# Optimization experiments

Hardware: AMD Instinct MI355X
Metric: run time of the kernel (lower is better)

Reference implementation:

```python
import jax, jax.numpy as jnp
import numpy as np


def setup_inputs() -> dict:
    key = jax.random.key(0)
    ks = jax.random.split(key, 5)
    N, C, H, W = 4, 256, 64, 64
    fan_scale = 1.0 / np.sqrt(C)  # kaiming-ish scale for 1x1 conv weights
    x = jax.random.normal(ks[0], (N, C, H, W), dtype=jnp.float32)
    Wq = jax.random.normal(ks[1], (C, C), dtype=jnp.float32) * fan_scale
    Wk = jax.random.normal(ks[2], (C, C), dtype=jnp.float32) * fan_scale
    Wv = jax.random.normal(ks[3], (C, C), dtype=jnp.float32) * fan_scale
    bq = jnp.zeros((C,), dtype=jnp.float32)
    bk = jnp.zeros((C,), dtype=jnp.float32)
    bv = jnp.zeros((C,), dtype=jnp.float32)
    gamma = jax.random.uniform(ks[4], (1,), dtype=jnp.float32)
    return {"x": x, "Wq": Wq, "bq": bq, "Wk": Wk, "bk": bk, "Wv": Wv, "bv": bv, "gamma": gamma}


def reference(x, Wq, bq, Wk, bk, Wv, bv, gamma):
    # x: (N, C, H, W); 1x1 convs are channel-mixing matmuls.
    N, C, H, W = x.shape
    HW = H * W
    xf = x.reshape(N, C, HW)
    q = jnp.einsum('oc,ncl->nol', Wq, xf) + bq[None, :, None]  # (N, C, HW)
    k = jnp.einsum('oc,ncl->nol', Wk, xf) + bk[None, :, None]
    v = jnp.einsum('oc,ncl->nol', Wv, xf) + bv[None, :, None]
    # spatial mode: energy = softmax(Q^T K) over last dim (no 1/sqrt(d) scaling)
    energy = jax.nn.softmax(jnp.einsum('nci,ncj->nij', q, k), axis=-1)  # (N, HW, HW)
    # att[n,c,i] = sum_j v[n,c,j] * energy[n,i,j]  (bmm(value, energy^T))
    att = jnp.einsum('ncj,nij->nci', v, energy)  # (N, C, HW)
    # in_channels == out_channels -> residual is identity
    out = x + gamma[0] * att.reshape(N, C, H, W)
    return out
```

## Files before the change

kernel.cpp:

```cpp
#include <hip/hip_runtime.h>

typedef unsigned short ushort_t;
typedef unsigned int u32;
typedef _Float16 f16;
typedef f16 f16x8 __attribute__((ext_vector_type(8)));
typedef f16 f16x2 __attribute__((ext_vector_type(2)));
typedef ushort_t u16x8 __attribute__((ext_vector_type(8)));
typedef float f32x4 __attribute__((ext_vector_type(4)));
typedef float f32x16 __attribute__((ext_vector_type(16)));

#define C_DIM 256
#define HW 4096
#define CHW (C_DIM*HW)
#define L2E 1.4426950408889634f

__device__ __align__(16) f16 g_xbT[4 * CHW];
__device__ __align__(16) f16 g_q[4 * CHW];
__device__ __align__(16) f16 g_k[4 * CHW];
__device__ __align__(16) f16 g_v[4 * CHW];
__device__ __align__(16) f16 g_opart[16 * CHW];
__device__ __align__(16) float g_ml[16 * 2 * HW];

__device__ __forceinline__ float bf2f(ushort_t h) {
    union { u32 u; float f; } v; v.u = ((u32)h) << 16; return v.f;
}
__device__ __forceinline__ ushort_t f2bf(float f) {
    union { float f; u32 u; } v; v.f = f;
    u32 r = v.u + 0x7FFF + ((v.u >> 16) & 1);
    return (ushort_t)(r >> 16);
}
__device__ __forceinline__ float fin0(float v) {
    return (v > -1e30f && v < 1e30f) ? v : 0.f;
}
__device__ __forceinline__ f16 sf16(float v) {
    return (f16)((v > -1e4f && v < 1e4f) ? v : 0.f);
}
__device__ __forceinline__ void gl2lds16(const f16* g, f16* l) {
    __builtin_amdgcn_global_load_lds(
        (const __attribute__((address_space(1))) u32*)g,
        (__attribute__((address_space(3))) u32*)l, 16, 0, 0);
}
__device__ __forceinline__ int probe_mode(const void* p) {
    int lane = threadIdx.x & 63;
    float v = fabsf(bf2f(((const ushort_t*)p)[lane]));
    v = (v < 1e6f) ? v : 1e6f;
#pragma unroll
    for (int d = 1; d < 64; d <<= 1) v += __shfl_xor(v, d, 64);
    return (v * (1.f / 64.f) > 100.f) ? 1 : 0;
}

__global__ void k_sentinel(ushort_t* out, int n) {
    int i = blockIdx.x * 256 + threadIdx.x;
    if (i < n) out[i] = f2bf(777.f);
}

__global__ __launch_bounds__(256) void k_transpose(const void* __restrict__ xv) {
    __shared__ f16 t[64][66];
    int mode = probe_mode(xv);
    int n = blockIdx.z, c0 = blockIdx.y * 64, l0 = blockIdx.x * 64;
    int tid = threadIdx.x;
    f16* ob = g_xbT + n * CHW;
    int lq = (tid & 15) * 4;
    int cl = tid >> 4;
    if (mode == 0) {
        const ushort_t* xb = (const ushort_t*)xv + n * CHW;
#pragma unroll
        for (int p = 0; p < 4; ++p) {
            int c = cl + 16 * p;
            ushort4 v = *(const ushort4*)(xb + (c0 + c) * HW + l0 + lq);
            t[lq + 0][c] = sf16(bf2f(v.x));
            t[lq + 1][c] = sf16(bf2f(v.y));
            t[lq + 2][c] = sf16(bf2f(v.z));
            t[lq + 3][c] = sf16(bf2f(v.w));
        }
    } else {
        const float* xb = (const float*)xv + n * CHW;
#pragma unroll
        for (int p = 0; p < 4; ++p) {
            int c = cl + 16 * p;
            float4 v = *(const float4*)(xb + (c0 + c) * HW + l0 + lq);
            t[lq + 0][c] = sf16(v.x);
            t[lq + 1][c] = sf16(v.y);
            t[lq + 2][c] = sf16(v.z);
            t[lq + 3][c] = sf16(v.w);
        }
    }
    __syncthreads();
    int c2 = (tid & 31) * 2;
    int lr = tid >> 5;
#pragma unroll
    for (int p = 0; p < 8; ++p) {
        int l = lr + 8 * p;
        u32 pair = *(const u32*)&t[l][c2];
        *(u32*)(ob + (l0 + l) * C_DIM + c0 + c2) = pair;
    }
}

__global__ __launch_bounds__(256) void k_proj(
    const void* __restrict__ Wq, const void* __restrict__ bq,
    const void* __restrict__ Wk, const void* __restrict__ bk,
    const void* __restrict__ Wv, const void* __restrict__ bv)
{
    __shared__ __align__(16) f16 lds_x[128 * 64];
    __shared__ __align__(16) f16 lds_w[128 * 64];
    int l0 = blockIdx.x * 128;
    int og0 = blockIdx.y * 128;
    int n = blockIdx.z;
    int mat = og0 >> 8;
    int om0 = og0 & 255;
    const void* W = (mat == 0) ? Wq : (mat == 1) ? Wk : Wv;
    const void* bias = (mat == 0) ? bq : (mat == 1) ? bk : bv;
    int mode = probe_mode(W);
    int tid = threadIdx.x, w = tid >> 6, lane = tid & 63;
    int quad = lane >> 4, l16 = lane & 15;
    const f16* xb = g_xbT + n * CHW;

    f32x4 acc[2][8];
#pragma unroll
    for (int a = 0; a < 2; a++)
#pragma unroll
        for (int b = 0; b < 8; b++) acc[a][b] = f32x4{0.f, 0.f, 0.f, 0.f};

    for (int ch = 0; ch < 4; ++ch) {
        int cc0 = ch * 64;
        f16x8 xs[4], wsr[4];
#pragma unroll
        for (int ti = 0; ti < 4; ++ti) {
            int s = (w * 4 + ti) * 64 + lane;
            int row = s >> 3, gp = s & 7;
            xs[ti] = *(const f16x8*)(xb + (l0 + row) * C_DIM + cc0 + gp * 8);
            f16x8 h;
            if (mode == 0) {
                u16x8 wv = *(const u16x8*)((const ushort_t*)W + (om0 + row) * C_DIM + cc0 + gp * 8);
#pragma unroll
                for (int e = 0; e < 8; e++) h[e] = sf16(bf2f(wv[e]));
            } else {
                const float* wf = (const float*)W + (om0 + row) * C_DIM + cc0 + gp * 8;
#pragma unroll
                for (int e = 0; e < 8; e++) h[e] = sf16(wf[e]);
            }
            wsr[ti] = h;
        }
        __syncthreads();
#pragma unroll
        for (int ti = 0; ti < 4; ++ti) {
            int s = (w * 4 + ti) * 64 + lane;
            int row = s >> 3, gp = s & 7;
            int pos = gp ^ (row & 7);
            *(f16x8*)(lds_x + (row * 8 + pos) * 8) = xs[ti];
            *(f16x8*)(lds_w + (row * 8 + pos) * 8) = wsr[ti];
        }
        __syncthreads();
#pragma unroll
        for (int ks = 0; ks < 2; ++ks) {
            f16x8 af[2];
#pragma unroll
            for (int mt = 0; mt < 2; ++mt) {
                int row = w * 32 + mt * 16 + l16;
                int g = ks * 4 + quad;
                int pos = g ^ (row & 7);
                af[mt] = *(const f16x8*)(lds_x + (row * 8 + pos) * 8);
            }
#pragma unroll
            for (int nt = 0; nt < 8; ++nt) {
                int rowo = nt * 16 + l16;
                int g = ks * 4 + quad;
                int pos = g ^ (rowo & 7);
                f16x8 bfv = *(const f16x8*)(lds_w + (rowo * 8 + pos) * 8);
                if (mat < 2) {
                    acc[0][nt] = __builtin_amdgcn_mfma_f32_16x16x32_f16(af[0], bfv, acc[0][nt], 0, 0, 0);
                    acc[1][nt] = __builtin_amdgcn_mfma_f32_16x16x32_f16(af[1], bfv, acc[1][nt], 0, 0, 0);
                } else {
                    acc[0][nt] = __builtin_amdgcn_mfma_f32_16x16x32_f16(bfv, af[0], acc[0][nt], 0, 0, 0);
                    acc[1][nt] = __builtin_amdgcn_mfma_f32_16x16x32_f16(bfv, af[1], acc[1][nt], 0, 0, 0);
                }
            }
        }
        __syncthreads();
    }

    auto loadb = [&](int i) -> float {
        return mode ? ((const float*)bias)[i] : bf2f(((const ushort_t*)bias)[i]);
    };
    if (mat < 2) {
        f16* T = ((mat == 0) ? g_q : g_k) + n * CHW;
        float bvv[8];
#pragma unroll
        for (int nt = 0; nt < 8; nt++) bvv[nt] = loadb(om0 + nt * 16 + l16);
#pragma unroll
        for (int mt = 0; mt < 2; mt++)
#pragma unroll
            for (int nt = 0; nt < 8; nt++)
#pragma unroll
                for (int r = 0; r < 4; r++) {
                    int l = l0 + w * 32 + mt * 16 + quad * 4 + r;
                    int o = om0 + nt * 16 + l16;
                    T[l * C_DIM + o] = sf16(acc[mt][nt][r] + bvv[nt]);
                }
    } else {
        f16* T = g_v + n * CHW;
#pragma unroll
        for (int mt = 0; mt < 2; mt++)
#pragma unroll
            for (int nt = 0; nt < 8; nt++)
#pragma unroll
                for (int r = 0; r < 4; r++) {
                    int o = om0 + nt * 16 + quad * 4 + r;
                    int l = l0 + w * 32 + mt * 16 + l16;
                    T[o * HW + l] = sf16(acc[mt][nt][r] + loadb(o));
                }
    }
}

__device__ __forceinline__ f16x8 pack_pfrag(const float* p, int h) {
    union PK { u32 u; f16x2 h2; } t0, t1, t2, t3;
    t0.h2 = f16x2{(f16)p[0], (f16)p[1]};
    t1.h2 = f16x2{(f16)p[2], (f16)p[3]};
    t2.h2 = f16x2{(f16)p[4], (f16)p[5]};
    t3.h2 = f16x2{(f16)p[6], (f16)p[7]};
    u32 sa = __shfl_xor(t0.u, 32, 64);
    u32 sb = __shfl_xor(t1.u, 32, 64);
    u32 sc = __shfl_xor(t2.u, 32, 64);
    u32 sd = __shfl_xor(t3.u, 32, 64);
    union RW { u32 w[4]; f16x8 v; } r;
    r.w[0] = h ? sc : t0.u;
    r.w[1] = h ? sd : t1.u;
    r.w[2] = h ? t2.u : sa;
    r.w[3] = h ? t3.u : sb;
    return r.v;
}

__global__ __launch_bounds__(256, 2) void k_attn() {
    __shared__ __align__(16) f16 smem[32768];
    f16* kbuf = smem;
    f16* vbuf = smem + 16384;

    int bid = blockIdx.x;
    int x8 = bid & 7;
    int n = x8 >> 1, jhi = x8 & 1;
    int rest = bid >> 3;
    int jlo = rest & 1;
    int i0 = (rest >> 1) * 128;
    int jq = jhi * 2 + jlo;
    int tid = threadIdx.x, w = tid >> 6, lane = tid & 63;
    int j5 = lane & 31, h = lane >> 5;

    const f16* Qb = g_q + n * CHW;
    const f16* Kb = g_k + n * CHW;
    const f16* Vb = g_v + n * CHW;

    f16x8 qf[16];
    {
        const f16* qrow = Qb + (i0 + w * 32 + j5) * C_DIM + h * 8;
#pragma unroll
        for (int ck = 0; ck < 16; ++ck)
            qf[ck] = *(const f16x8*)(qrow + ck * 16);
    }

    int k_lane = h * 256 + j5 * 8;
    int v_lane = h * 2048 + j5 * 8;

    const f16* ksrc = Kb + (jq * 1024 + j5) * C_DIM + (w * 2 + h) * 8;
    const f16* vsrc = Vb + tid * HW + jq * 1024;
    int dst_w = w * 512;

    f32x16 o_acc[8];
#pragma unroll
    for (int ct = 0; ct < 8; ++ct)
#pragma unroll
        for (int r = 0; r < 16; ++r) o_acc[ct][r] = 0.f;

    float m_ = -1e30f, l_ = 0.f, al_prev = 1.f;
    f16x8 pf0 = {}, pf1 = {};

#pragma unroll
    for (int s = 0; s < 4; ++s) gl2lds16(ksrc + s * 64, kbuf + s * 2048 + dst_w);
    ksrc += 32 * C_DIM;
    __syncthreads();

    for (int it = 0; it < 32; ++it) {
        int kcur = it & 1;
        if (it < 31) {
#pragma unroll
            for (int s = 0; s < 4; ++s)
                gl2lds16(ksrc + s * 64, kbuf + (kcur ^ 1) * 8192 + s * 2048 + dst_w);
            ksrc += 32 * C_DIM;
        }
#pragma unroll
        for (int s = 0; s < 4; ++s)
            gl2lds16(vsrc + s * 8, vbuf + (it & 1) * 8192 + s * 2048 + dst_w);
        vsrc += 32;

        if (it > 0 && __any(al_prev < 1.f)) {
#pragma unroll
            for (int ct = 0; ct < 8; ++ct)
#pragma unroll
                for (int r = 0; r < 16; ++r) o_acc[ct][r] *= al_prev;
        }

        const f16* kb = kbuf + kcur * 8192 + k_lane;
        f32x16 sa, sb;
#pragma unroll
        for (int r = 0; r < 16; ++r) { sa[r] = 0.f; sb[r] = 0.f; }
        __builtin_amdgcn_s_setprio(1);
        if (it > 0) {
            const f16* vb = vbuf + ((it - 1) & 1) * 8192 + v_lane;
#pragma unroll
            for (int ck = 0; ck < 16; ++ck) {
                f16x8 kf = *(const f16x8*)(kb + ck * 512);
                if (ck & 1) sb = __builtin_amdgcn_mfma_f32_32x32x16_f16(kf, qf[ck], sb, 0, 0, 0);
                else        sa = __builtin_amdgcn_mfma_f32_32x32x16_f16(kf, qf[ck], sa, 0, 0, 0);
                f16x8 vf = *(const f16x8*)(vb + (ck & 1) * 4096 + (ck >> 1) * 256);
                o_acc[ck >> 1] = __builtin_amdgcn_mfma_f32_32x32x16_f16(
                    vf, (ck & 1) ? pf1 : pf0, o_acc[ck >> 1], 0, 0, 0);
            }
        } else {
#pragma unroll
            for (int ck = 0; ck < 16; ++ck) {
                f16x8 kf = *(const f16x8*)(kb + ck * 512);
                if (ck & 1) sb = __builtin_amdgcn_mfma_f32_32x32x16_f16(kf, qf[ck], sb, 0, 0, 0);
                else        sa = __builtin_amdgcn_mfma_f32_32x32x16_f16(kf, qf[ck], sa, 0, 0, 0);
            }
        }
        __builtin_amdgcn_s_setprio(0);
        f32x16 st;
#pragma unroll
        for (int r = 0; r < 16; ++r) st[r] = sa[r] + sb[r];

        float mx0 = fmaxf(fmaxf(st[0], st[1]), fmaxf(st[2], st[3]));
        float mx1 = fmaxf(fmaxf(st[4], st[5]), fmaxf(st[6], st[7]));
        float mx2 = fmaxf(fmaxf(st[8], st[9]), fmaxf(st[10], st[11]));
        float mx3 = fmaxf(fmaxf(st[12], st[13]), fmaxf(st[14], st[15]));
        float smax = fmaxf(fmaxf(mx0, mx1), fmaxf(mx2, mx3));
        smax = fmaxf(smax, __shfl_xor(smax, 32, 64));
        float mq = __builtin_ceilf(smax * 0.125f) * 8.f;
        float mn = fmaxf(m_, mq);
        float al = __builtin_amdgcn_exp2f((m_ - mn) * L2E);
        float nl = -mn * L2E;
        float p[16];
#pragma unroll
        for (int r = 0; r < 16; ++r)
            p[r] = __builtin_amdgcn_exp2f(st[r] * L2E + nl);
        float a0 = (p[0] + p[1]) + (p[2] + p[3]);
        float a1 = (p[4] + p[5]) + (p[6] + p[7]);
        float a2 = (p[8] + p[9]) + (p[10] + p[11]);
        float a3 = (p[12] + p[13]) + (p[14] + p[15]);
        float rs = (a0 + a1) + (a2 + a3);
        m_ = mn;
        l_ = l_ * al + rs;
        al_prev = al;
        pf0 = pack_pfrag(p, h);
        pf1 = pack_pfrag(p + 8, h);

        __syncthreads();
    }

    {
        if (__any(al_prev < 1.f)) {
#pragma unroll
            for (int ct = 0; ct < 8; ++ct)
#pragma unroll
                for (int r = 0; r < 16; ++r) o_acc[ct][r] *= al_prev;
        }
        const f16* vb = vbuf + 8192 + v_lane;
#pragma unroll
        for (int ct = 0; ct < 8; ++ct) {
            f16x8 v0 = *(const f16x8*)(vb + ct * 256);
            f16x8 v1 = *(const f16x8*)(vb + 4096 + ct * 256);
            o_acc[ct] = __builtin_amdgcn_mfma_f32_32x32x16_f16(v0, pf0, o_acc[ct], 0, 0, 0);
            o_acc[ct] = __builtin_amdgcn_mfma_f32_32x32x16_f16(v1, pf1, o_acc[ct], 0, 0, 0);
        }
    }

    l_ += __shfl_xor(l_, 32, 64);

    int slot = jq * 4 + n;
    int i_out = i0 + w * 32 + j5;
    if (h == 0) {
        g_ml[(slot * 2 + 0) * HW + i_out] = m_;
        g_ml[(slot * 2 + 1) * HW + i_out] = l_;
    }
    float inv = (l_ > 1e-30f) ? 1.f / l_ : 0.f;
    f16* ob = g_opart + slot * CHW + i_out;
#pragma unroll
    for (int ct = 0; ct < 8; ++ct) {
        int cbase = ct * 32 + 4 * h;
#pragma unroll
        for (int r = 0; r < 16; ++r) {
            int c = cbase + (r & 3) + 8 * (r >> 2);
            ob[c * HW] = (f16)(o_acc[ct][r] * inv);
        }
    }
}

__global__ __launch_bounds__(256) void k_combine(
    const void* __restrict__ xv, const void* __restrict__ gv, void* __restrict__ outv)
{
    int mode = probe_mode(xv);
    float gam = fin0(mode ? ((const float*)gv)[0] : bf2f(((const ushort_t*)gv)[0]));
    int n = blockIdx.y;
    int off = blockIdx.x * 2048 + threadIdx.x * 8;
    int i = off & (HW - 1);

    u16x8 op[4];
    float ms[4][8], ls[4][8];
#pragma unroll
    for (int s = 0; s < 4; ++s) {
        int slot = s * 4 + n;
        op[s] = *(const u16x8*)((const ushort_t*)g_opart + slot * CHW + off);
        float4 mA = *(const float4*)&g_ml[(slot * 2 + 0) * HW + i];
        float4 mB = *(const float4*)&g_ml[(slot * 2 + 0) * HW + i + 4];
        float4 lA = *(const float4*)&g_ml[(slot * 2 + 1) * HW + i];
        float4 lB = *(const float4*)&g_ml[(slot * 2 + 1) * HW + i + 4];
        ms[s][0]=mA.x; ms[s][1]=mA.y; ms[s][2]=mA.z; ms[s][3]=mA.w;
        ms[s][4]=mB.x; ms[s][5]=mB.y; ms[s][6]=mB.z; ms[s][7]=mB.w;
        ls[s][0]=lA.x; ls[s][1]=lA.y; ls[s][2]=lA.z; ls[s][3]=lA.w;
        ls[s][4]=lB.x; ls[s][5]=lB.y; ls[s][6]=lB.z; ls[s][7]=lB.w;
    }

    float o[8];
#pragma unroll
    for (int e = 0; e < 8; ++e) {
        float m = fmaxf(fmaxf(ms[0][e], ms[1][e]), fmaxf(ms[2][e], ms[3][e]));
        float num = 0.f, den = 0.f;
#pragma unroll
        for (int s = 0; s < 4; ++s) {
            float wgt = __builtin_amdgcn_exp2f((ms[s][e] - m) * L2E) * ls[s][e];
            union { ushort_t u; f16 h; } cv; cv.u = (ushort_t)op[s][e];
            num += wgt * (float)cv.h;
            den += wgt;
        }
        o[e] = (den > 1e-30f) ? num / den : 0.f;
    }

    if (mode == 0) {
        u16x8 xp = *(const u16x8*)((const ushort_t*)xv + n * CHW + off);
        u16x8 res;
#pragma unroll
        for (int e = 0; e < 8; ++e)
            res[e] = f2bf(fin0(bf2f((ushort_t)xp[e]) + gam * o[e]));
        *(u16x8*)((ushort_t*)outv + n * CHW + off) = res;
    } else {
        const float* xb = (const float*)xv + n * CHW + off;
        float* outb = (float*)outv + n * CHW + off;
        float4 xA = *(const float4*)xb;
        float4 xB = *(const float4*)(xb + 4);
        float4 rA, rB;
        rA.x = fin0(xA.x + gam * o[0]); rA.y = fin0(xA.y + gam * o[1]);
        rA.z = fin0(xA.z + gam * o[2]); rA.w = fin0(xA.w + gam * o[3]);
        rB.x = fin0(xB.x + gam * o[4]); rB.y = fin0(xB.y + gam * o[5]);
        rB.z = fin0(xB.z + gam * o[6]); rB.w = fin0(xB.w + gam * o[7]);
        *(float4*)outb = rA;
        *(float4*)(outb + 4) = rB;
    }
}

extern "C" void kernel_launch(void* const* d_in, const int* in_sizes, int n_in,
                              void* d_out, int out_size, void* d_ws, size_t ws_size,
                              hipStream_t stream) {
    (void)d_ws; (void)ws_size;
    bool ok = (n_in == 8) &&
              in_sizes[0] == 4 * CHW &&
              in_sizes[1] == C_DIM * C_DIM && in_sizes[2] == C_DIM &&
              in_sizes[3] == C_DIM * C_DIM && in_sizes[4] == C_DIM &&
              in_sizes[5] == C_DIM * C_DIM && in_sizes[6] == C_DIM &&
              in_sizes[7] == 1 && out_size == 4 * CHW;
    if (!ok) {
        hipLaunchKernelGGL(k_sentinel, dim3((out_size + 255) / 256), dim3(256), 0, stream,
                           (ushort_t*)d_out, out_size);
        return;
    }
    hipLaunchKernelGGL(k_transpose, dim3(64, 4, 4), dim3(256), 0, stream, d_in[0]);
    hipLaunchKernelGGL(k_proj, dim3(32, 6, 4), dim3(256), 0, stream,
                       d_in[1], d_in[2], d_in[3], d_in[4], d_in[5], d_in[6]);
    hipLaunchKernelGGL(k_attn, dim3(512), dim3(256), 0, stream);
    hipLaunchKernelGGL(k_combine, dim3(CHW / 2048, 4), dim3(256), 0, stream,
                       d_in[0], d_in[7], d_out);
}
```

Before: 239.3 us.

## Restructure flash-attention loop with split barriers and explicit vmcnt waits

Replaces the single end-of-iteration __syncthreads with two explicit s_barrier points, each using a partial s_waitcnt vmcnt so newer global-to-LDS K/V copies can stay in flight while older ones are consumed. The PV MFMAs move out of the interleaved QK loop into a separate block placed after the mid-iteration barrier, and the last iteration is peeled. The aim is to stop draining all outstanding loads at every barrier and so overlap memory traffic with compute better. It relies on hand-counted vmcnt values and sched_barriers, which are fragile if the number of loads per thread changes, and it loses the previous interleaving of QK and PV MFMAs.

```diff
diff --git a/kernel.cpp b/kernel.cpp
--- a/kernel.cpp
+++ b/kernel.cpp
@@ -276,56 +276,61 @@
 #pragma unroll
     for (int s = 0; s < 4; ++s) gl2lds16(ksrc + s * 64, kbuf + s * 2048 + dst_w);
     ksrc += 32 * C_DIM;
-    __syncthreads();
-
-    for (int it = 0; it < 32; ++it) {
+    asm volatile("s_waitcnt vmcnt(0)" ::: "memory");
+    __builtin_amdgcn_s_barrier();
+    __builtin_amdgcn_sched_barrier(0);
+
+    for (int it = 0; it < 31; ++it) {
         int kcur = it & 1;
-        if (it < 31) {
-#pragma unroll
-            for (int s = 0; s < 4; ++s)
-                gl2lds16(ksrc + s * 64, kbuf + (kcur ^ 1) * 8192 + s * 2048 + dst_w);
-            ksrc += 32 * C_DIM;
-        }
 #pragma unroll
         for (int s = 0; s < 4; ++s)
-            gl2lds16(vsrc + s * 8, vbuf + (it & 1) * 8192 + s * 2048 + dst_w);
+            gl2lds16(ksrc + s * 64, kbuf + (kcur ^ 1) * 8192 + s * 2048 + dst_w);
+        ksrc += 32 * C_DIM;
+        __builtin_amdgcn_sched_barrier(0);
+#pragma unroll
+        for (int s = 0; s < 4; ++s)
+            gl2lds16(vsrc + s * 8, vbuf + kcur * 8192 + s * 2048 + dst_w);
         vsrc += 32;
-
-        if (it > 0 && __any(al_prev < 1.f)) {
-#pragma unroll
-            for (int ct = 0; ct < 8; ++ct)
-#pragma unroll
-                for (int r = 0; r < 16; ++r) o_acc[ct][r] *= al_prev;
-        }
+        __builtin_amdgcn_sched_barrier(0);
 
         const f16* kb = kbuf + kcur * 8192 + k_lane;
         f32x16 sa, sb;
 #pragma unroll
         for (int r = 0; r < 16; ++r) { sa[r] = 0.f; sb[r] = 0.f; }
         __builtin_amdgcn_s_setprio(1);
-        if (it > 0) {
-            const f16* vb = vbuf + ((it - 1) & 1) * 8192 + v_lane;
-#pragma unroll
-            for (int ck = 0; ck < 16; ++ck) {
-                f16x8 kf = *(const f16x8*)(kb + ck * 512);
-                if (ck & 1) sb = __builtin_amdgcn_mfma_f32_32x32x16_f16(kf, qf[ck], sb, 0, 0, 0);
-                else        sa = __builtin_amdgcn_mfma_f32_32x32x16_f16(kf, qf[ck], sa, 0, 0, 0);
-                f16x8 vf = *(const f16x8*)(vb + (ck & 1) * 4096 + (ck >> 1) * 256);
-                o_acc[ck >> 1] = __builtin_amdgcn_mfma_f32_32x32x16_f16(
-                    vf, (ck & 1) ? pf1 : pf0, o_acc[ck >> 1], 0, 0, 0);
-            }
-        } else {
-#pragma unroll
-            for (int ck = 0; ck < 16; ++ck) {
-                f16x8 kf = *(const f16x8*)(kb + ck * 512);
-                if (ck & 1) sb = __builtin_amdgcn_mfma_f32_32x32x16_f16(kf, qf[ck], sb, 0, 0, 0);
-                else        sa = __builtin_amdgcn_mfma_f32_32x32x16_f16(kf, qf[ck], sa, 0, 0, 0);
-            }
+#pragma unroll
+        for (int ck = 0; ck < 16; ++ck) {
+            f16x8 kf = *(const f16x8*)(kb + ck * 512);
+            if (ck & 1) sb = __builtin_amdgcn_mfma_f32_32x32x16_f16(kf, qf[ck], sb, 0, 0, 0);
+            else        sa = __builtin_amdgcn_mfma_f32_32x32x16_f16(kf, qf[ck], sa, 0, 0, 0);
         }
         __builtin_amdgcn_s_setprio(0);
         f32x16 st;
 #pragma unroll
         for (int r = 0; r < 16; ++r) st[r] = sa[r] + sb[r];
+
+        asm volatile("s_waitcnt vmcnt(8)" ::: "memory");
+        __builtin_amdgcn_s_barrier();
+        __builtin_amdgcn_sched_barrier(0);
+
+        if (it > 0) {
+            if (__any(al_prev < 1.f)) {
+#pragma unroll
+                for (int ct = 0; ct < 8; ++ct)
+#pragma unroll
+                    for (int r = 0; r < 16; ++r) o_acc[ct][r] *= al_prev;
+            }
+            const f16* vb = vbuf + (kcur ^ 1) * 8192 + v_lane;
+            __builtin_amdgcn_s_setprio(1);
+#pragma unroll
+            for (int ct = 0; ct < 8; ++ct) {
+                f16x8 v0 = *(const f16x8*)(vb + ct * 256);
+                f16x8 v1 = *(const f16x8*)(vb + 4096 + ct * 256);
+                o_acc[ct] = __builtin_amdgcn_mfma_f32_32x32x16_f16(v0, pf0, o_acc[ct], 0, 0, 0);
+                o_acc[ct] = __builtin_amdgcn_mfma_f32_32x32x16_f16(v1, pf1, o_acc[ct], 0, 0, 0);
+            }
+            __builtin_amdgcn_s_setprio(0);
+        }
 
         float mx0 = fmaxf(fmaxf(st[0], st[1]), fmaxf(st[2], st[3]));
         float mx1 = fmaxf(fmaxf(st[4], st[5]), fmaxf(st[6], st[7]));
@@ -352,10 +357,84 @@
         pf0 = pack_pfrag(p, h);
         pf1 = pack_pfrag(p + 8, h);
 
-        __syncthreads();
+        asm volatile("s_waitcnt vmcnt(4)" ::: "memory");
+        __builtin_amdgcn_s_barrier();
+        __builtin_amdgcn_sched_barrier(0);
     }
 
     {
+#pragma unroll
+        for (int s = 0; s < 4; ++s)
+            gl2lds16(vsrc + s * 8, vbuf + 8192 + s * 2048 + dst_w);
+        __builtin_amdgcn_sched_barrier(0);
+
+        const f16* kb = kbuf + 8192 + k_lane;
+        f32x16 sa, sb;
+#pragma unroll
+        for (int r = 0; r < 16; ++r) { sa[r] = 0.f; sb[r] = 0.f; }
+        __builtin_amdgcn_s_setprio(1);
+#pragma unroll
+        for (int ck = 0; ck < 16; ++ck) {
+            f16x8 kf = *(const f16x8*)(kb + ck * 512);
+            if (ck & 1) sb = __builtin_amdgcn_mfma_f32_32x32x16_f16(kf, qf[ck], sb, 0, 0, 0);
+            else        sa = __builtin_amdgcn_mfma_f32_32x32x16_f16(kf, qf[ck], sa, 0, 0, 0);
+        }
+        __builtin_amdgcn_s_setprio(0);
+        f32x16 st;
+#pragma unroll
+        for (int r = 0; r < 16; ++r) st[r] = sa[r] + sb[r];
+
+        asm volatile("s_waitcnt vmcnt(4)" ::: "memory");
+        __builtin_amdgcn_s_barrier();
+        __builtin_amdgcn_sched_barrier(0);
+
+        if (__any(al_prev < 1.f)) {
+#pragma unroll
+            for (int ct = 0; ct < 8; ++ct)
+#pragma unroll
+                for (int r = 0; r < 16; ++r) o_acc[ct][r] *= al_prev;
+        }
+        {
+            const f16* vb = vbuf + v_lane;
+            __builtin_amdgcn_s_setprio(1);
+#pragma unroll
+            for (int ct = 0; ct < 8; ++ct) {
+                f16x8 v0 = *(const f16x8*)(vb + ct * 256);
+                f16x8 v1 = *(const f16x8*)(vb + 4096 + ct * 256);
+                o_acc[ct] = __builtin_amdgcn_mfma_f32_32x32x16_f16(v0, pf0, o_acc[ct], 0, 0, 0);
+                o_acc[ct] = __builtin_amdgcn_mfma_f32_32x32x16_f16(v1, pf1, o_acc[ct], 0, 0, 0);
+            }
+            __builtin_amdgcn_s_setprio(0);
+        }
+        float mx0 = fmaxf(fmaxf(st[0], st[1]), fmaxf(st[2], st[3]));
+        float mx1 = fmaxf(fmaxf(st[4], st[5]), fmaxf(st[6], st[7]));
+        float mx2 = fmaxf(fmaxf(st[8], st[9]), fmaxf(st[10], st[11]));
+        float mx3 = fmaxf(fmaxf(st[12], st[13]), fmaxf(st[14], st[15]));
+        float smax = fmaxf(fmaxf(mx0, mx1), fmaxf(mx2, mx3));
+        smax = fmaxf(smax, __shfl_xor(smax, 32, 64));
+        float mq = __builtin_ceilf(smax * 0.125f) * 8.f;
+        float mn = fmaxf(m_, mq);
+        float al = __builtin_amdgcn_exp2f((m_ - mn) * L2E);
+        float nl = -mn * L2E;
+        float p[16];
+#pragma unroll
+        for (int r = 0; r < 16; ++r)
+            p[r] = __builtin_amdgcn_exp2f(st[r] * L2E + nl);
+        float a0 = (p[0] + p[1]) + (p[2] + p[3]);
+        float a1 = (p[4] + p[5]) + (p[6] + p[7]);
+        float a2 = (p[8] + p[9]) + (p[10] + p[11]);
+        float a3 = (p[12] + p[13]) + (p[14] + p[15]);
+        float rs = (a0 + a1) + (a2 + a3);
+        m_ = mn;
+        l_ = l_ * al + rs;
+        al_prev = al;
+        pf0 = pack_pfrag(p, h);
+        pf1 = pack_pfrag(p + 8, h);
+
+        asm volatile("s_waitcnt vmcnt(0)" ::: "memory");
+        __builtin_amdgcn_s_barrier();
+        __builtin_amdgcn_sched_barrier(0);
+
         if (__any(al_prev < 1.f)) {
 #pragma unroll
             for (int ct = 0; ct < 8; ++ct)
```

New measurement: 240.1 us. About the same (+0.3%).
